# Kernel optimization log

Measured on AMD Instinct MI355X. Metric: run time of the kernel, lower is better.

The kernel has to match this reference:

```python
import jax, jax.numpy as jnp
import numpy as np

DIM = 1024
NUM_HEADS = 16
HEAD_DIM = DIM // NUM_HEADS
SCALE = 1.0 / np.sqrt(HEAD_DIM)
B, S = 2, 2048


def setup_inputs() -> dict:
    key = jax.random.key(0)
    ks = jax.random.split(key, 10)
    std = 1.0 / np.sqrt(DIM)
    return {
        "x": jax.random.normal(ks[0], (B, S, DIM), dtype=jnp.float32),
        "Wq": jax.random.normal(ks[1], (DIM, DIM), dtype=jnp.float32) * std,
        "bq": jnp.zeros((DIM,), dtype=jnp.float32),
        "Wk": jax.random.normal(ks[2], (DIM, DIM), dtype=jnp.float32) * std,
        "bk": jnp.zeros((DIM,), dtype=jnp.float32),
        "Wv": jax.random.normal(ks[3], (DIM, DIM), dtype=jnp.float32) * std,
        "bv": jnp.zeros((DIM,), dtype=jnp.float32),
        "Wo": jax.random.normal(ks[4], (DIM, DIM), dtype=jnp.float32) * std,
        "bo": jnp.zeros((DIM,), dtype=jnp.float32),
        "mobius_weight": jax.random.normal(ks[5], (1,), dtype=jnp.float32) * 0.01,
    }


def _split_heads(t):
    b, s, _ = t.shape
    return t.reshape(b, s, NUM_HEADS, HEAD_DIM).transpose(0, 2, 1, 3)  # bhsd


def reference(x, Wq, bq, Wk, bk, Wv, bv, Wo, bo, mobius_weight):
    q = _split_heads(x @ Wq.T + bq)
    k = _split_heads(x @ Wk.T + bk)
    v = _split_heads(x @ Wv.T + bv)

    # similarity: plain QK^T
    similarity = jnp.einsum('bhqd,bhkd->bhqk', q, k)
    # mobius cross-term: q_omega . k_pi + q_pi . k_omega
    h = HEAD_DIM // 2
    q_om, q_pi = q[..., :h], q[..., h:]
    k_om, k_pi = k[..., :h], k[..., h:]
    mobius = jnp.einsum('bhqd,bhkd->bhqk', q_om, k_pi) + \
             jnp.einsum('bhqd,bhkd->bhqk', q_pi, k_om)

    incidence = (similarity + mobius_weight[0] * mobius) * SCALE
    attn = jax.nn.softmax(incidence, axis=-1)
    out = jnp.einsum('bhqk,bhkd->bhqd', attn, v)
    out = out.transpose(0, 2, 1, 3).reshape(x.shape[0], x.shape[1], DIM)
    return out @ Wo.T + bo
```

## Files before the change

kernel.cpp:

```cpp
#include <hip/hip_runtime.h>


typedef __attribute__((ext_vector_type(8))) short short8;
typedef __attribute__((ext_vector_type(4))) short s16x4;
typedef __attribute__((ext_vector_type(4))) float f32x4;
typedef __attribute__((ext_vector_type(16))) float f32x16;
typedef __attribute__((ext_vector_type(8))) __bf16 bf16x8;
typedef __attribute__((ext_vector_type(4))) unsigned uint4v;

__device__ __forceinline__ float exp2fa(float x) {
  return __builtin_amdgcn_exp2f(x);
}
__device__ __forceinline__ short f2bf(float f) {
  unsigned u = __builtin_bit_cast(unsigned, f);
  u = u + 0x7fffu + ((u >> 16) & 1u);
  return (short)(u >> 16);
}
__device__ __forceinline__ f32x4 mfma16(bf16x8 a, bf16x8 b, f32x4 c) {
  return __builtin_amdgcn_mfma_f32_16x16x32_bf16(a, b, c, 0, 0, 0);
}
__device__ __forceinline__ f32x16 mfma32(bf16x8 a, bf16x8 b, f32x16 c) {
  return __builtin_amdgcn_mfma_f32_32x32x16_bf16(a, b, c, 0, 0, 0);
}
__device__ __forceinline__ void gload_lds16(const void* g, void* l) {
  __builtin_amdgcn_global_load_lds(
      (const __attribute__((address_space(1))) unsigned int*)g,
      (__attribute__((address_space(3))) unsigned int*)l, 16, 0, 0);
}
__device__ __forceinline__ unsigned pkbf(float a, float b) {
  unsigned r;
  asm("v_cvt_pk_bf16_f32 %0, %1, %2" : "=v"(r) : "v"(a), "v"(b));
  return r;
}
__device__ __forceinline__ void plswap(unsigned& a, unsigned& b) {
  asm volatile("v_permlane32_swap_b32 %0, %1" : "+v"(a), "+v"(b));
}
__device__ __forceinline__ bf16x8 pack8(float x0, float x1, float x2, float x3,
                                        float x4, float x5, float x6, float x7) {
  unsigned a0 = pkbf(x0, x1), a1 = pkbf(x2, x3);
  unsigned a2 = pkbf(x4, x5), a3 = pkbf(x6, x7);
  plswap(a0, a2);
  plswap(a1, a3);
  uint4v u = {a0, a1, a2, a3};
  return __builtin_bit_cast(bf16x8, u);
}

__global__ void cast_all_kernel(const float* x, const float* w0, const float* w1,
                                const float* w2, const float* w3, short* xo,
                                short* o0, short* o1, short* o2, short* o3) {
  const float* in; short* out;
  const int r = blockIdx.y;
  size_t off;
  if (r < 4) { in = x; out = xo; off = (size_t)r * 131072; }
  else {
    switch (r) {
      case 4: in = w0; out = o0; break;
      case 5: in = w1; out = o1; break;
      case 6: in = w2; out = o2; break;
      default: in = w3; out = o3; break;
    }
    off = 0;
  }
  const size_t i = off + blockIdx.x * 256 + threadIdx.x;
  const float4* p = (const float4*)in;
  float4 a = p[2 * i], b = p[2 * i + 1];
  short8 o;
  o[0] = f2bf(a.x); o[1] = f2bf(a.y); o[2] = f2bf(a.z); o[3] = f2bf(a.w);
  o[4] = f2bf(b.x); o[5] = f2bf(b.y); o[6] = f2bf(b.z); o[7] = f2bf(b.w);
  ((short8*)out)[i] = o;
}

constexpr int GK = 1024, GN = 1024;
constexpr float QSCALE = 0.125f * 1.44269504088896340736f;

template <int EP>
__device__ __forceinline__ void gemm_body(char* lds, const short* __restrict__ A,
                                          const short* __restrict__ W,
                                          const float* __restrict__ bias,
                                          void* __restrict__ C,
                                          const float* __restrict__ mwp) {
  const int tid = threadIdx.x;
  const int l = tid & 63, w = tid >> 6;
  const int wr = w >> 1, wc = w & 1;
  const int m0 = blockIdx.y * 128, n0 = blockIdx.x * 128;

  f32x4 acc[4][4] = {};

  const int rg = l >> 3, c8 = l & 7;
  for (int kb = 0; kb < GK / 64; ++kb) {
    const int k0 = kb * 64;
#pragma unroll
    for (int i = 0; i < 4; ++i) {
      const int ra = i * 32 + w * 8 + rg;
      gload_lds16(A + (size_t)(m0 + ra) * GK + k0 + ((c8 ^ (ra & 7)) * 8),
                  lds + (i * 32 + w * 8) * 128);
      gload_lds16(W + (size_t)(n0 + ra) * GK + k0 + ((c8 ^ (ra & 7)) * 8),
                  lds + 16384 + (i * 32 + w * 8) * 128);
    }
    __syncthreads();
#pragma unroll
    for (int ks = 0; ks < 2; ++ks) {
      bf16x8 af[4], bfr[4];
      const int chunk = ks * 4 + (l >> 4);
#pragma unroll
      for (int mf = 0; mf < 4; ++mf) {
        const int mt = wr * 64 + mf * 16 + (l & 15);
        af[mf] = *(const bf16x8*)(lds + mt * 128 + ((chunk ^ (mt & 7)) * 16));
      }
#pragma unroll
      for (int nf = 0; nf < 4; ++nf) {
        const int nt = wc * 64 + nf * 16 + (l & 15);
        bfr[nf] = *(const bf16x8*)(lds + 16384 + nt * 128 + ((chunk ^ (nt & 7)) * 16));
      }
#pragma unroll
      for (int mf = 0; mf < 4; ++mf)
#pragma unroll
        for (int nf = 0; nf < 4; ++nf)
          acc[mf][nf] = mfma16(af[mf], bfr[nf], acc[mf][nf]);
    }
    __syncthreads();
  }

  const float mwv = (EP == 1) ? mwp[0] : 0.f;
#pragma unroll
  for (int mf = 0; mf < 4; ++mf)
#pragma unroll
    for (int nf = 0; nf < 4; ++nf) {
      const int n = n0 + wc * 64 + nf * 16 + (l & 15);
      const int mb = m0 + wr * 64 + mf * 16 + (l >> 4) * 4;
      if (EP == 2) {
        s16x4 v;
#pragma unroll
        for (int r = 0; r < 4; ++r) v[r] = f2bf(acc[mf][nf][r] + bias[n]);
        const int b = mb >> 11, s0 = mb & 2047;
        *(s16x4*)((short*)C + ((size_t)(b * 1024 + n)) * 2048 + s0) = v;
      } else {
        const float bv = bias[n];
#pragma unroll
        for (int r = 0; r < 4; ++r) {
          const int m = mb + r;
          float v = acc[mf][nf][r] + bv;
          if (EP == 0) v *= QSCALE;
          if (EP == 1) v += mwv * (acc[mf][nf ^ 2][r] + bias[n ^ 32]);
          if (EP == 3)
            ((float*)C)[(size_t)m * GN + n] = v;
          else
            ((short*)C)[(size_t)m * GN + n] = f2bf(v);
        }
      }
    }
}

__global__ __launch_bounds__(256) void gemm_qkv_kernel(
    const short* __restrict__ A, const short* Wq, const short* Wk, const short* Wv,
    const float* bq, const float* bk, const float* bv, short* q, short* kt,
    short* vt, const float* mw) {
  __shared__ __align__(16) char lds[32768];
  if (blockIdx.z == 0) gemm_body<0>(lds, A, Wq, bq, q, nullptr);
  else if (blockIdx.z == 1) gemm_body<1>(lds, A, Wk, bk, kt, mw);
  else gemm_body<2>(lds, A, Wv, bv, vt, nullptr);
}

__global__ __launch_bounds__(256) void gemm_out_kernel(const short* __restrict__ A,
                                                       const short* __restrict__ W,
                                                       const float* __restrict__ bias,
                                                       float* __restrict__ C) {
  __shared__ __align__(16) char lds[32768];
  gemm_body<3>(lds, A, W, bias, C, nullptr);
}

__global__ __launch_bounds__(256) void attn_kernel(const short* __restrict__ Q,
                                                   const short* __restrict__ K,
                                                   const short* __restrict__ VT,
                                                   short* __restrict__ O) {
  constexpr int S = 2048;
  constexpr float FM = 16.0f;
  __shared__ __align__(16) char lds[2][16384];
  const int tid = threadIdx.x;
  const int l = tid & 63, w = tid >> 6;
  const int lo = l & 31, hi = l >> 5;
  const int bh = blockIdx.y, b = bh >> 4, h = bh & 15;
  const int q0 = blockIdx.x * 128 + w * 32;
  const size_t base = (size_t)b * S * 1024 + h * 64;
  const size_t vtrow0 = (size_t)(b * 1024 + h * 64);

  bf16x8 qf[4];
  {
    const short* qp = Q + base + (size_t)(q0 + lo) * 1024 + hi * 8;
#pragma unroll
    for (int ds = 0; ds < 4; ++ds) qf[ds] = *(const bf16x8*)(qp + ds * 16);
  }

  f32x16 o0 = {}, o1 = {};
  float lrow = 0.f;

  const int srow = tid >> 3, sc8 = tid & 7;
  auto STAGE = [&](int kt, int bb) {
    char* Kd = lds[bb];
    char* Vd = lds[bb] + 8192;
    const int k0 = kt * 64;
#pragma unroll
    for (int p = 0; p < 2; ++p) {
      const int row = p * 32 + srow;
      gload_lds16(K + base + (size_t)(k0 + row) * 1024 + ((sc8 ^ (row & 7)) * 8),
                  Kd + p * 4096 + w * 1024);
      gload_lds16(VT + (vtrow0 + row) * 2048 + k0 + ((sc8 ^ (row & 7)) * 8),
                  Vd + p * 4096 + w * 1024);
    }
  };

  auto TILE = [&](const char* Kb, const char* Vb) {
    f32x16 st0, st1;
#pragma unroll
    for (int r = 0; r < 16; ++r) { st0[r] = -FM; st1[r] = -FM; }
    __builtin_amdgcn_s_setprio(1);
#pragma unroll
    for (int ds = 0; ds < 4; ++ds) {
      const int c = ds * 2 + hi;
      bf16x8 kf0 = *(const bf16x8*)(Kb + lo * 128 + ((c ^ (lo & 7)) * 16));
      bf16x8 kf1 = *(const bf16x8*)(Kb + (32 + lo) * 128 + ((c ^ (lo & 7)) * 16));
      st0 = mfma32(kf0, qf[ds], st0);
      st1 = mfma32(kf1, qf[ds], st1);
    }
    __builtin_amdgcn_s_setprio(0);

#pragma unroll
    for (int r = 0; r < 16; ++r) st0[r] = exp2fa(st0[r]);
#pragma unroll
    for (int r = 0; r < 16; ++r) st1[r] = exp2fa(st1[r]);
    float ts[8];
#pragma unroll
    for (int r = 0; r < 8; ++r)
      ts[r] = (st0[r] + st0[r + 8]) + (st1[r] + st1[r + 8]);
#pragma unroll
    for (int d = 4; d >= 1; d >>= 1)
#pragma unroll
      for (int r = 0; r < 4; ++r)
        if (r < d) ts[r] += ts[r + d];
    lrow += ts[0] + __shfl_xor(ts[0], 32);

    bf16x8 pf[4];
    pf[0] = pack8(st0[0], st0[1], st0[2], st0[3], st0[4], st0[5], st0[6], st0[7]);
    pf[1] = pack8(st0[8], st0[9], st0[10], st0[11], st0[12], st0[13], st0[14], st0[15]);
    pf[2] = pack8(st1[0], st1[1], st1[2], st1[3], st1[4], st1[5], st1[6], st1[7]);
    pf[3] = pack8(st1[8], st1[9], st1[10], st1[11], st1[12], st1[13], st1[14], st1[15]);

    __builtin_amdgcn_s_setprio(1);
#pragma unroll
    for (int kv = 0; kv < 4; ++kv) {
      const int c = kv * 2 + hi;
      bf16x8 vf0 = *(const bf16x8*)(Vb + lo * 128 + ((c ^ (lo & 7)) * 16));
      bf16x8 vf1 = *(const bf16x8*)(Vb + (32 + lo) * 128 + ((c ^ (lo & 7)) * 16));
      o0 = mfma32(vf0, pf[kv], o0);
      o1 = mfma32(vf1, pf[kv], o1);
    }
    __builtin_amdgcn_s_setprio(0);
  };

  STAGE(0, 0);
  for (int kt = 0; kt < S / 64; kt += 2) {
    STAGE(kt + 1, 1);
    asm volatile("s_waitcnt vmcnt(4)" ::: "memory");
    __builtin_amdgcn_s_barrier();
    TILE(lds[0], lds[0] + 8192);
    asm volatile("" ::: "memory");
    __builtin_amdgcn_s_barrier();

    if (kt + 2 < S / 64) {
      STAGE(kt + 2, 0);
      asm volatile("s_waitcnt vmcnt(4)" ::: "memory");
    } else {
      asm volatile("s_waitcnt vmcnt(0)" ::: "memory");
    }
    __builtin_amdgcn_s_barrier();
    TILE(lds[1], lds[1] + 8192);
    asm volatile("" ::: "memory");
    __builtin_amdgcn_s_barrier();
  }

  const float inv = 1.0f / lrow;
  short* Op = O + base + (size_t)(q0 + lo) * 1024;
#pragma unroll
  for (int g = 0; g < 4; ++g) {
    s16x4 v0, v1;
#pragma unroll
    for (int r = 0; r < 4; ++r) {
      v0[r] = f2bf(o0[g * 4 + r] * inv);
      v1[r] = f2bf(o1[g * 4 + r] * inv);
    }
    *(s16x4*)(Op + 8 * g + 4 * hi) = v0;
    *(s16x4*)(Op + 32 + 8 * g + 4 * hi) = v1;
  }
}

extern "C" void kernel_launch(void* const* d_in, const int* in_sizes, int n_in,
                              void* d_out, int out_size, void* d_ws, size_t ws_size,
                              hipStream_t stream) {
  const float* x  = (const float*)d_in[0];
  const float* Wq = (const float*)d_in[1];
  const float* bq = (const float*)d_in[2];
  const float* Wk = (const float*)d_in[3];
  const float* bk = (const float*)d_in[4];
  const float* Wv = (const float*)d_in[5];
  const float* bv = (const float*)d_in[6];
  const float* Wo = (const float*)d_in[7];
  const float* bo = (const float*)d_in[8];
  const float* mw = (const float*)d_in[9];
  float* out = (float*)d_out;
  char* ws = (char*)d_ws;
  const size_t MB = (size_t)1 << 20;

  short* xb  = (short*)(ws + 0 * MB);
  short* wqb = (short*)(ws + 8 * MB);
  short* wkb = (short*)(ws + 10 * MB);
  short* wvb = (short*)(ws + 12 * MB);
  short* wob = (short*)(ws + 14 * MB);
  short* qb  = (short*)(ws + 16 * MB);
  short* ktb = (short*)(ws + 24 * MB);
  short* vtb = (short*)(ws + 32 * MB);
  short* ob  = (short*)(ws + 40 * MB);

  cast_all_kernel<<<dim3(512, 8), 256, 0, stream>>>(x, Wq, Wk, Wv, Wo, xb, wqb,
                                                    wkb, wvb, wob);
  gemm_qkv_kernel<<<dim3(8, 32, 3), 256, 0, stream>>>(xb, wqb, wkb, wvb, bq, bk, bv,
                                                      qb, ktb, vtb, mw);
  attn_kernel<<<dim3(16, 32), 256, 0, stream>>>(qb, ktb, vtb, ob);
  gemm_out_kernel<<<dim3(8, 32), 256, 0, stream>>>(ob, wob, bo, out);
}
```

Baseline: 128.7 us.

## Split attention KV loop across two wave groups with LDS reduction

The attention block now runs 8 waves (512 threads) instead of 4. The two wave groups each process alternating 64-key tiles of the same 128 queries, staged through a 4-deep LDS ring, then combine partial outputs and row sums through LDS before normalizing. The softmax uses a fixed max offset, so plain addition of the partials is valid. This doubles the waves per block to hide latency and halves each wave's serial KV loop. The cost is doubled LDS, an extra reduction phase, and higher register pressure under launch_bounds(512,4).

```diff
diff --git a/kernel.cpp b/kernel.cpp
--- a/kernel.cpp
+++ b/kernel.cpp
@@ -169,18 +169,19 @@
   gemm_body<3>(lds, A, W, bias, C, nullptr);
 }
 
-__global__ __launch_bounds__(256) void attn_kernel(const short* __restrict__ Q,
-                                                   const short* __restrict__ K,
-                                                   const short* __restrict__ VT,
-                                                   short* __restrict__ O) {
+__global__ __launch_bounds__(512, 4) void attn_kernel(const short* __restrict__ Q,
+                                                      const short* __restrict__ K,
+                                                      const short* __restrict__ VT,
+                                                      short* __restrict__ O) {
   constexpr int S = 2048;
   constexpr float FM = 16.0f;
-  __shared__ __align__(16) char lds[2][16384];
+  __shared__ __align__(16) char lds[4][16384];
   const int tid = threadIdx.x;
   const int l = tid & 63, w = tid >> 6;
+  const int grp = w >> 2, w4 = w & 3;
   const int lo = l & 31, hi = l >> 5;
   const int bh = blockIdx.y, b = bh >> 4, h = bh & 15;
-  const int q0 = blockIdx.x * 128 + w * 32;
+  const int q0 = blockIdx.x * 128 + w4 * 32;
   const size_t base = (size_t)b * S * 1024 + h * 64;
   const size_t vtrow0 = (size_t)(b * 1024 + h * 64);
 
@@ -195,17 +196,17 @@
   float lrow = 0.f;
 
   const int srow = tid >> 3, sc8 = tid & 7;
-  auto STAGE = [&](int kt, int bb) {
-    char* Kd = lds[bb];
-    char* Vd = lds[bb] + 8192;
-    const int k0 = kt * 64;
-#pragma unroll
-    for (int p = 0; p < 2; ++p) {
-      const int row = p * 32 + srow;
-      gload_lds16(K + base + (size_t)(k0 + row) * 1024 + ((sc8 ^ (row & 7)) * 8),
-                  Kd + p * 4096 + w * 1024);
-      gload_lds16(VT + (vtrow0 + row) * 2048 + k0 + ((sc8 ^ (row & 7)) * 8),
-                  Vd + p * 4096 + w * 1024);
+  auto STAGE = [&](int pr) {
+#pragma unroll
+    for (int g2 = 0; g2 < 2; ++g2) {
+      const int t = 2 * pr + g2;
+      char* Kd = lds[t & 3];
+      char* Vd = lds[t & 3] + 8192;
+      const int k0 = t * 64;
+      gload_lds16(K + base + (size_t)(k0 + srow) * 1024 + ((sc8 ^ (srow & 7)) * 8),
+                  Kd + w * 1024);
+      gload_lds16(VT + (vtrow0 + srow) * 2048 + k0 + ((sc8 ^ (srow & 7)) * 8),
+                  Vd + w * 1024);
     }
   };
 
@@ -257,39 +258,61 @@
     __builtin_amdgcn_s_setprio(0);
   };
 
-  STAGE(0, 0);
-  for (int kt = 0; kt < S / 64; kt += 2) {
-    STAGE(kt + 1, 1);
-    asm volatile("s_waitcnt vmcnt(4)" ::: "memory");
-    __builtin_amdgcn_s_barrier();
-    TILE(lds[0], lds[0] + 8192);
-    asm volatile("" ::: "memory");
-    __builtin_amdgcn_s_barrier();
-
-    if (kt + 2 < S / 64) {
-      STAGE(kt + 2, 0);
+  STAGE(0);
+  for (int p = 0; p < S / 128; ++p) {
+    if (p < S / 128 - 1) {
+      STAGE(p + 1);
       asm volatile("s_waitcnt vmcnt(4)" ::: "memory");
     } else {
       asm volatile("s_waitcnt vmcnt(0)" ::: "memory");
     }
     __builtin_amdgcn_s_barrier();
-    TILE(lds[1], lds[1] + 8192);
+    const char* buf = lds[(2 * p + grp) & 3];
+    TILE(buf, buf + 8192);
     asm volatile("" ::: "memory");
     __builtin_amdgcn_s_barrier();
   }
 
-  const float inv = 1.0f / lrow;
-  short* Op = O + base + (size_t)(q0 + lo) * 1024;
-#pragma unroll
-  for (int g = 0; g < 4; ++g) {
-    s16x4 v0, v1;
-#pragma unroll
-    for (int r = 0; r < 4; ++r) {
-      v0[r] = f2bf(o0[g * 4 + r] * inv);
-      v1[r] = f2bf(o1[g * 4 + r] * inv);
-    }
-    *(s16x4*)(Op + 8 * g + 4 * hi) = v0;
-    *(s16x4*)(Op + 32 + 8 * g + 4 * hi) = v1;
+  __syncthreads();
+  float* mbuf = (float*)&lds[0][0];
+  float* lbuf = (float*)&lds[2][0];
+  if (grp == 1) {
+#pragma unroll
+    for (int g = 0; g < 4; ++g) {
+      const int c0 = (2 * g + hi) ^ (lo & 15);
+      const int c1 = (8 + 2 * g + hi) ^ (lo & 15);
+      f32x4 v0, v1;
+#pragma unroll
+      for (int r = 0; r < 4; ++r) { v0[r] = o0[g * 4 + r]; v1[r] = o1[g * 4 + r]; }
+      *(f32x4*)(mbuf + (w4 * 32 + lo) * 64 + c0 * 4) = v0;
+      *(f32x4*)(mbuf + (w4 * 32 + lo) * 64 + c1 * 4) = v1;
+    }
+    if (hi == 0) lbuf[w4 * 32 + lo] = lrow;
+  }
+  __syncthreads();
+  if (grp == 0) {
+#pragma unroll
+    for (int g = 0; g < 4; ++g) {
+      const int c0 = (2 * g + hi) ^ (lo & 15);
+      const int c1 = (8 + 2 * g + hi) ^ (lo & 15);
+      f32x4 v0 = *(const f32x4*)(mbuf + (w4 * 32 + lo) * 64 + c0 * 4);
+      f32x4 v1 = *(const f32x4*)(mbuf + (w4 * 32 + lo) * 64 + c1 * 4);
+#pragma unroll
+      for (int r = 0; r < 4; ++r) { o0[g * 4 + r] += v0[r]; o1[g * 4 + r] += v1[r]; }
+    }
+    const float inv = 1.0f / (lrow + lbuf[w4 * 32 + lo]);
+    short* Op = O + base + (size_t)(q0 + lo) * 1024;
+#pragma unroll
+    for (int g = 0; g < 4; ++g) {
+      s16x4 v0, v1;
+#pragma unroll
+      for (int r = 0; r < 4; ++r) {
+        v0[r] = f2bf(o0[g * 4 + r] * inv);
+        v1[r] = f2bf(o1[g * 4 + r] * inv);
+      }
+      *(s16x4*)(Op + 8 * g + 4 * hi) = v0;
+      *(s16x4*)(Op + 32 + 8 * g + 4 * hi) = v1;
+    }
   }
 }
 
@@ -324,6 +347,6 @@
                                                     wkb, wvb, wob);
   gemm_qkv_kernel<<<dim3(8, 32, 3), 256, 0, stream>>>(xb, wqb, wkb, wvb, bq, bk, bv,
                                                       qb, ktb, vtb, mw);
-  attn_kernel<<<dim3(16, 32), 256, 0, stream>>>(qb, ktb, vtb, ob);
+  attn_kernel<<<dim3(16, 32), 512, 0, stream>>>(qb, ktb, vtb, ob);
   gemm_out_kernel<<<dim3(8, 32), 256, 0, stream>>>(ob, wob, bo, out);
 }
```

Measured after the change: 131.9 us. +2.5%, slower.
